# Optimization experiments

Hardware: AMD Instinct MI355X
Metric: run time of the kernel (lower is better)

## Reference

```python
import jax, jax.numpy as jnp
import numpy as np

B, L, D_MODEL = 2, 2048, 2048
D_INNER, D_STATE, D_CONV, DT_RANK = 4096, 16, 4, 128


def setup_inputs() -> dict:
    key = jax.random.key(0)
    ks = jax.random.split(key, 8)
    s = 0.02
    return {
        "hidden_states": jax.random.normal(ks[0], (B, L, D_MODEL), jnp.float32),
        "in_proj_weight": jax.random.normal(ks[1], (2 * D_INNER, D_MODEL), jnp.float32) * s,
        "conv1d_weight": jax.random.normal(ks[2], (D_INNER, 1, D_CONV), jnp.float32) * s,
        "conv1d_bias": jnp.zeros((D_INNER,), jnp.float32),
        "x_proj_weight": jax.random.normal(ks[3], (DT_RANK + 2 * D_STATE, D_INNER), jnp.float32) * s,
        "dt_proj_weight": jax.random.normal(ks[4], (D_INNER, DT_RANK), jnp.float32) * s,
        "dt_proj_bias": jax.random.uniform(ks[5], (D_INNER,), jnp.float32, -4.0, -2.0),
        "out_proj_weight": jax.random.normal(ks[6], (D_MODEL, D_INNER), jnp.float32) * s,
        # real Mamba init: A_log = log(1..d_state) broadcast over channels
        "A_log": jnp.log(jnp.broadcast_to(jnp.arange(1, D_STATE + 1, dtype=jnp.float32), (D_INNER, D_STATE))),
        "D": jnp.ones((D_INNER,), jnp.float32),
    }


def reference(hidden_states, in_proj_weight, conv1d_weight, conv1d_bias,
              x_proj_weight, dt_proj_weight, dt_proj_bias, out_proj_weight,
              A_log, D):
    negA = -jnp.exp(A_log)  # [d_inner, d_state]
    # in_proj (no bias) then transpose(1,2): [B, 2*d_inner, L]
    xz = jnp.einsum('bld,ed->bel', hidden_states, in_proj_weight)
    x, z = jnp.split(xz, 2, axis=1)  # each [B, d_inner, L]
    # causal depthwise conv1d + silu
    x = jax.lax.conv_general_dilated(
        x, conv1d_weight, window_strides=(1,), padding=[(D_CONV - 1, 0)],
        dimension_numbers=('NCH', 'OIH', 'NCH'), feature_group_count=D_INNER,
    ) + conv1d_bias[None, :, None]
    x = jax.nn.silu(x)
    xT = x.transpose(0, 2, 1)  # [B, L, d_inner]
    # x_proj -> (dt_rank, d_state, d_state)
    x_dbl = jnp.einsum('bld,ed->ble', xT, x_proj_weight)
    dt_lo = x_dbl[..., :DT_RANK]
    Bm = x_dbl[..., DT_RANK:DT_RANK + D_STATE]   # [B, L, n]
    Cm = x_dbl[..., DT_RANK + D_STATE:]          # [B, L, n]
    # dt_proj + delta_bias, softplus (delta_softplus=True)
    dt = jax.nn.softplus(jnp.einsum('blr,dr->bld', dt_lo, dt_proj_weight) + dt_proj_bias)

    # selective scan: h_t = exp(dt_t*A)*h_{t-1} + dt_t*x_t*B_t ; y_t = C_t . h_t
    def step(h, inp):
        dt_t, B_t, C_t, x_t = inp  # [B,d],[B,n],[B,n],[B,d]
        dA = jnp.exp(dt_t[..., None] * negA)           # [B, d, n]
        h = h * dA + (dt_t * x_t)[..., None] * B_t[:, None, :]
        y = jnp.einsum('bdn,bn->bd', h, C_t)
        return h, y

    h0 = jnp.zeros((B, D_INNER, D_STATE), dt.dtype)
    _, ys = jax.lax.scan(
        step, h0,
        (dt.transpose(1, 0, 2), Bm.transpose(1, 0, 2),
         Cm.transpose(1, 0, 2), xT.transpose(1, 0, 2)),
    )  # ys: [L, B, d_inner]
    y = ys.transpose(1, 0, 2) + xT * D          # skip connection D*x
    y = y * jax.nn.silu(z.transpose(0, 2, 1))   # gate
    # out_proj (no bias): [B, L, d_model]
    return jnp.einsum('bld,ed->ble', y, out_proj_weight)
```

## Files before the change

kernel.cpp:

```cpp
#include <hip/hip_runtime.h>
#include <math.h>

#define B_ 2
#define L_ 2048
#define DMODEL 2048
#define DINNER 4096
#define DSTATE 16
#define DCONV 4
#define DTRANK 128
#define NCHUNK 32
#define CLEN 64
#define MROWS 4096

typedef unsigned short ushort_t;
typedef unsigned int uint_t;
typedef __attribute__((ext_vector_type(8))) short bf16x8;
typedef __attribute__((ext_vector_type(4))) float floatx4;

__device__ __forceinline__ float sigmoidf_(float x){ return 1.f/(1.f+__expf(-x)); }
__device__ __forceinline__ ushort_t f2bf(float f){
    uint_t u = __builtin_bit_cast(uint_t, f);
    return (ushort_t)((u + 0x7FFFu + ((u >> 16) & 1u)) >> 16);
}
__device__ __forceinline__ float bf2f(ushort_t h){
    return __builtin_bit_cast(float, (uint_t)h << 16);
}
__device__ __forceinline__ float fast_exp2(float x){
#if __has_builtin(__builtin_amdgcn_exp2f)
    return __builtin_amdgcn_exp2f(x);
#else
    return exp2f(x);
#endif
}
#define LOG2E 1.44269504088896f

#define GLD_LDS16(g, l) __builtin_amdgcn_global_load_lds( \
    (const __attribute__((address_space(1))) void*)(g),   \
    (__attribute__((address_space(3))) void*)(l), 16, 0, 0)

template<int OUTBF, int EPI, int SPLIT, int KSPLIT>
__global__ __launch_bounds__(256)
void gemm_mfma(const ushort_t* __restrict__ Aptr, int lda,
               const ushort_t* __restrict__ W, int ldw,
               void* __restrict__ Cptr, void* __restrict__ C2,
               int ldc, int Klen,
               const float* __restrict__ bias)
{
    __shared__ ushort_t lsA[128*64];
    __shared__ ushort_t lsW[128*64];
    const int tid  = threadIdx.x;
    const int row0 = blockIdx.x * 128;
    const int col0 = blockIdx.y * 128;
    const int koff = KSPLIT ? blockIdx.z * Klen : 0;
    const int lane = tid & 63;
    const int wv   = tid >> 6;
    const int wm   = (wv >> 1) * 64;
    const int wn   = (wv & 1) * 64;
    const int lr   = lane & 15;
    const int lq   = lane >> 4;

    floatx4 acc[4][4];
    #pragma unroll
    for(int i=0;i<4;i++)
        #pragma unroll
        for(int j=0;j<4;j++)
            #pragma unroll
            for(int r=0;r<4;r++) acc[i][j][r] = 0.f;

    for(int k0 = koff; k0 < koff + Klen; k0 += 64){
        #pragma unroll
        for(int it=0; it<4; it++){
            const int slot = it*256 + tid;
            const int row  = slot >> 3;
            const int p    = slot & 7;
            const int s    = p ^ (row & 7);
            const ushort_t* gw = W    + (size_t)(col0 + row)*ldw + k0 + s*8;
            const ushort_t* ga = Aptr + (size_t)(row0 + row)*lda + k0 + s*8;
            GLD_LDS16(gw, &lsW[slot*8]);
            GLD_LDS16(ga, &lsA[slot*8]);
        }
        __syncthreads();

        #pragma unroll
        for(int kk=0; kk<2; kk++){
            bf16x8 af[4], bw[4];
            #pragma unroll
            for(int i=0;i<4;i++){
                const int ra = wm + i*16 + lr;
                const int rb = wn + i*16 + lr;
                af[i] = *(const bf16x8*)&lsA[ra*64 + (((kk*4+lq) ^ (ra&7))*8)];
                bw[i] = *(const bf16x8*)&lsW[rb*64 + (((kk*4+lq) ^ (rb&7))*8)];
            }
            #pragma unroll
            for(int i=0;i<4;i++)
                #pragma unroll
                for(int j=0;j<4;j++)
                    acc[i][j] = __builtin_amdgcn_mfma_f32_16x16x32_bf16(af[i], bw[j], acc[i][j], 0, 0, 0);
        }
        __syncthreads();
    }

    void* dst = Cptr;
    int cbase = col0;
    if (SPLIT && col0 >= ldc){ dst = C2; cbase = col0 - ldc; }
    const size_t zoff = KSPLIT ? (size_t)blockIdx.z * MROWS * ldc : 0;

    #pragma unroll
    for(int i=0;i<4;i++){
        #pragma unroll
        for(int r=0;r<4;r++){
            const int row = row0 + wm + i*16 + lq*4 + r;
            #pragma unroll
            for(int j=0;j<4;j++){
                const int col = cbase + wn + j*16 + lr;
                float v = acc[i][j][r];
                if (EPI){
                    v += bias[col];
                    v = (v > 20.f) ? v : log1pf(expf(v));
                }
                if (OUTBF) ((ushort_t*)dst)[(size_t)row*ldc + col] = f2bf(v);
                else       ((float*)  dst)[zoff + (size_t)row*ldc + col] = v;
            }
        }
    }
}

__global__ __launch_bounds__(256)
void cvt_bf16(const float* __restrict__ in, ushort_t* __restrict__ out, int n4)
{
    const int i = blockIdx.x*256 + threadIdx.x;
    if (i < n4){
        float4 v = *(const float4*)(in + (size_t)i*4);
        union { ushort_t u[4]; uint2 q; } p;
        p.u[0]=f2bf(v.x); p.u[1]=f2bf(v.y); p.u[2]=f2bf(v.z); p.u[3]=f2bf(v.w);
        *(uint2*)(out + (size_t)i*4) = p.q;
    }
}

__global__ __launch_bounds__(256)
void cvt_pad256(const float* __restrict__ in, ushort_t* __restrict__ out)
{
    const int i = blockIdx.x*256 + threadIdx.x;
    const int row = i >> 10;
    const int c4  = i & 1023;
    union { ushort_t u[4]; uint2 q; } p;
    if (row < 160){
        float4 v = *(const float4*)(in + (size_t)row*4096 + c4*4);
        p.u[0]=f2bf(v.x); p.u[1]=f2bf(v.y); p.u[2]=f2bf(v.z); p.u[3]=f2bf(v.w);
    } else { p.u[0]=0; p.u[1]=0; p.u[2]=0; p.u[3]=0; }
    *(uint2*)(out + (size_t)i*4) = p.q;
}

__global__ __launch_bounds__(256)
void reduce_xproj(const float* __restrict__ P, float* __restrict__ xdbl,
                  ushort_t* __restrict__ dtlo)
{
    const int row = blockIdx.x;
    const int col = threadIdx.x;
    float s = 0.f;
    #pragma unroll
    for(int z=0; z<8; z++)
        s += P[(size_t)z*MROWS*256 + (size_t)row*256 + col];
    if (col < 160) xdbl[(size_t)row*160 + col] = s;
    if (col < DTRANK) dtlo[(size_t)row*DTRANK + col] = f2bf(s);
}

__global__ __launch_bounds__(256)
void conv_silu_bf(const ushort_t* __restrict__ xb, const float* __restrict__ w,
                  const float* __restrict__ bias, ushort_t* __restrict__ xc)
{
    const int gid = blockIdx.x*256 + threadIdx.x;
    const int d = gid & (DINNER-1);
    const int t = gid >> 12;
    const int l = t & (L_-1);
    float s = bias[d];
    #pragma unroll
    for(int j=0;j<DCONV;j++){
        const int ll = l - (DCONV-1) + j;
        if (ll >= 0)
            s = fmaf(bf2f(xb[(size_t)(t-(DCONV-1)+j)*DINNER + d]), w[d*DCONV+j], s);
    }
    xc[(size_t)t*DINNER + d] = f2bf(s * sigmoidf_(s));
}

__global__ __launch_bounds__(256)
void scan_phase1(const ushort_t* __restrict__ dt_bf,
                 const ushort_t* __restrict__ xconv,
                 const float* __restrict__ xdbl,
                 const float* __restrict__ A_log,
                 float* __restrict__ sc_h, float* __restrict__ sc_S)
{
    const int tid = threadIdx.x;
    const int d = blockIdx.x*256 + tid;
    const int chunk = blockIdx.y;
    const int b = blockIdx.z;
    const int l0 = chunk*CLEN;

    __shared__ float Bs[CLEN][DSTATE];
    for(int i=tid; i<CLEN*DSTATE; i+=256){
        const int row = i >> 4, n = i & 15;
        Bs[row][n] = xdbl[(size_t)(b*L_ + l0 + row)*160 + DTRANK + n];
    }
    float negA[DSTATE];
    #pragma unroll
    for(int n=0;n<DSTATE;n++) negA[n] = -expf(A_log[d*DSTATE + n]) * LOG2E;
    __syncthreads();

    float h[DSTATE], S[DSTATE];
    #pragma unroll
    for(int n=0;n<DSTATE;n++){ h[n]=0.f; S[n]=0.f; }

    size_t idx = (size_t)(b*L_ + l0)*DINNER + d;
    float dt_c = bf2f(dt_bf[idx]);
    float xv_c = bf2f(xconv[idx]);
    for(int l=0;l<CLEN;l++){
        float dt_n = 0.f, xv_n = 0.f;
        if (l+1 < CLEN){
            dt_n = bf2f(dt_bf[idx + DINNER]);
            xv_n = bf2f(xconv[idx + DINNER]);
        }
        const float dx = dt_c * xv_c;
        #pragma unroll
        for(int n=0;n<DSTATE;n++){
            const float t = dt_c * negA[n];
            S[n] += t;
            h[n] = fmaf(h[n], fast_exp2(t), dx*Bs[l][n]);
        }
        dt_c = dt_n; xv_c = xv_n;
        idx += DINNER;
    }
    const size_t o = (size_t)(b*NCHUNK + chunk)*DSTATE*DINNER + d;
    #pragma unroll
    for(int n=0;n<DSTATE;n++){
        sc_h[o + (size_t)n*DINNER] = h[n];
        sc_S[o + (size_t)n*DINNER] = S[n];
    }
}

__global__ __launch_bounds__(256)
void scan_phase2(float* __restrict__ sc_h, const float* __restrict__ sc_S)
{
    const int gid = blockIdx.x*256 + threadIdx.x;
    const int b = gid / (DSTATE*DINNER);
    const int rem = gid - b*DSTATE*DINNER;
    const size_t base = (size_t)b*NCHUNK*DSTATE*DINNER + rem;
    float H = 0.f;
    #pragma unroll
    for(int c=0;c<NCHUNK;c++){
        const size_t idx = base + (size_t)c*DSTATE*DINNER;
        const float he = sc_h[idx];
        const float S  = sc_S[idx];
        sc_h[idx] = H;
        H = fmaf(fast_exp2(S), H, he);
    }
}

__global__ __launch_bounds__(256)
void scan_phase3(const ushort_t* __restrict__ dt_bf,
                 const ushort_t* __restrict__ xconv,
                 const float* __restrict__ xdbl,
                 const ushort_t* __restrict__ z_bf,
                 const float* __restrict__ A_log,
                 const float* __restrict__ Dvec,
                 const float* __restrict__ sc_h,
                 ushort_t* __restrict__ y_bf)
{
    const int tid = threadIdx.x;
    const int d = blockIdx.x*256 + tid;
    const int chunk = blockIdx.y;
    const int b = blockIdx.z;
    const int l0 = chunk*CLEN;

    __shared__ float BCs[CLEN][2*DSTATE];
    for(int i=tid; i<CLEN*2*DSTATE; i+=256){
        const int row = i >> 5, c = i & 31;
        BCs[row][c] = xdbl[(size_t)(b*L_ + l0 + row)*160 + DTRANK + c];
    }
    float negA[DSTATE];
    #pragma unroll
    for(int n=0;n<DSTATE;n++) negA[n] = -expf(A_log[d*DSTATE + n]) * LOG2E;
    const float Dv = Dvec[d];
    float h[DSTATE];
    const size_t o = (size_t)(b*NCHUNK + chunk)*DSTATE*DINNER + d;
    #pragma unroll
    for(int n=0;n<DSTATE;n++) h[n] = sc_h[o + (size_t)n*DINNER];
    __syncthreads();

    size_t idx = (size_t)(b*L_ + l0)*DINNER + d;
    float dt_c = bf2f(dt_bf[idx]);
    float xv_c = bf2f(xconv[idx]);
    float zv_c = bf2f(z_bf[idx]);
    for(int l=0;l<CLEN;l++){
        float dt_n = 0.f, xv_n = 0.f, zv_n = 0.f;
        if (l+1 < CLEN){
            dt_n = bf2f(dt_bf[idx + DINNER]);
            xv_n = bf2f(xconv[idx + DINNER]);
            zv_n = bf2f(z_bf[idx + DINNER]);
        }
        const float dx = dt_c * xv_c;
        float y = 0.f;
        #pragma unroll
        for(int n=0;n<DSTATE;n++){
            const float t = dt_c * negA[n];
            h[n] = fmaf(h[n], fast_exp2(t), dx*BCs[l][n]);
            y = fmaf(h[n], BCs[l][DSTATE+n], y);
        }
        const float g = zv_c * sigmoidf_(zv_c);
        y_bf[idx] = f2bf(fmaf(xv_c, Dv, y) * g);
        dt_c = dt_n; xv_c = xv_n; zv_c = zv_n;
        idx += DINNER;
    }
}

extern "C" void kernel_launch(void* const* d_in, const int* in_sizes, int n_in,
                              void* d_out, int out_size, void* d_ws, size_t ws_size,
                              hipStream_t stream) {
    const float* hs      = (const float*)d_in[0];
    const float* w_in    = (const float*)d_in[1];
    const float* w_conv  = (const float*)d_in[2];
    const float* b_conv  = (const float*)d_in[3];
    const float* w_xproj = (const float*)d_in[4];
    const float* w_dt    = (const float*)d_in[5];
    const float* b_dt    = (const float*)d_in[6];
    const float* w_out   = (const float*)d_in[7];
    const float* A_log   = (const float*)d_in[8];
    const float* Dvec    = (const float*)d_in[9];
    float* out = (float*)d_out;

    char* base = (char*)d_ws;
    ushort_t* x_bf   = (ushort_t*)(base);
    float*    xdbl   = (float*)   (base);
    ushort_t* wx_bf  = (ushort_t*)(base + (4u<<20));
    ushort_t* dtlo_bf= (ushort_t*)(base + (6u<<20));
    ushort_t* wdt_bf = (ushort_t*)(base + (7u<<20));
    float*    sc_h   = (float*)   (base + (8u<<20));
    ushort_t* z_bf   = (ushort_t*)(base + (32u<<20));
    ushort_t* xconv  = (ushort_t*)(base + (64u<<20));
    ushort_t* wi_bf  = (ushort_t*)(base + (96u<<20));
    ushort_t* dt_bf  = (ushort_t*)(base + (96u<<20));
    ushort_t* hs_bf  = (ushort_t*)(base + (128u<<20));
    float*    sc_S   = (float*)   (base + (128u<<20));
    ushort_t* wo_bf  = (ushort_t*)(base + (128u<<20));
    float*    xp_par = (float*)   (base + (144u<<20));
    ushort_t* y_bf   = (ushort_t*)(base + (144u<<20));

    dim3 blk(256);

    cvt_bf16<<<dim3(MROWS*DMODEL/4/256), blk, 0, stream>>>(hs, hs_bf, MROWS*DMODEL/4);
    cvt_bf16<<<dim3(2*DINNER*DMODEL/4/256), blk, 0, stream>>>(w_in, wi_bf, 2*DINNER*DMODEL/4);

    gemm_mfma<1,0,1,0><<<dim3(MROWS/128, 2*DINNER/128), blk, 0, stream>>>(
        hs_bf, DMODEL, wi_bf, DMODEL, x_bf, z_bf, DINNER, DMODEL, nullptr);

    conv_silu_bf<<<dim3((size_t)MROWS*DINNER/256), blk, 0, stream>>>(x_bf, w_conv, b_conv, xconv);

    cvt_pad256<<<dim3(256*4096/4/256), blk, 0, stream>>>(w_xproj, wx_bf);
    gemm_mfma<0,0,0,1><<<dim3(MROWS/128, 2, 8), blk, 0, stream>>>(
        xconv, DINNER, wx_bf, DINNER, xp_par, nullptr, 256, DINNER/8, nullptr);
    reduce_xproj<<<dim3(MROWS), blk, 0, stream>>>(xp_par, xdbl, dtlo_bf);

    cvt_bf16<<<dim3(DINNER*DTRANK/4/256), blk, 0, stream>>>(w_dt, wdt_bf, DINNER*DTRANK/4);
    gemm_mfma<1,1,0,0><<<dim3(MROWS/128, DINNER/128), blk, 0, stream>>>(
        dtlo_bf, DTRANK, wdt_bf, DTRANK, dt_bf, nullptr, DINNER, DTRANK, b_dt);

    dim3 sgrid(DINNER/256, NCHUNK, B_);
    scan_phase1<<<sgrid, blk, 0, stream>>>(dt_bf, xconv, xdbl, A_log, sc_h, sc_S);
    scan_phase2<<<dim3(B_*DSTATE*DINNER/256), blk, 0, stream>>>(sc_h, sc_S);

    cvt_bf16<<<dim3(DMODEL*DINNER/4/256), blk, 0, stream>>>(w_out, wo_bf, DMODEL*DINNER/4);

    scan_phase3<<<sgrid, blk, 0, stream>>>(dt_bf, xconv, xdbl, z_bf, A_log, Dvec, sc_h, y_bf);

    gemm_mfma<0,0,0,0><<<dim3(MROWS/128, DMODEL/128), blk, 0, stream>>>(
        y_bf, DINNER, wo_bf, DINNER, out, nullptr, DMODEL, DINNER, nullptr);
}
```

Before: 669.7 us.

## Use 256x256-tile 512-thread MFMA GEMM for in_proj and split-K out_proj

Adds a new GEMM kernel with 256x256 output tiles, 512 threads, double-buffered direct global-to-LDS loads, swizzled LDS layout and priority-boosted MFMA phases. It replaces the 128x128 GEMM for in_proj and for out_proj. The out_proj uses split-K by 2 into a float partial buffer, followed by a reduction kernel. The aim is more data reuse per tile and better latency hiding. In exchange it adds register pressure, an extra partial-sum write and read for out_proj, and one more launch.

```diff
diff --git a/kernel.cpp b/kernel.cpp
--- a/kernel.cpp
+++ b/kernel.cpp
@@ -125,6 +125,175 @@
     }
 }
 
+template<int OUTBF, int SPLIT, int KSPLIT>
+__global__ __launch_bounds__(512, 2)
+void gemm_256(const ushort_t* __restrict__ Aptr, int lda,
+              const ushort_t* __restrict__ W, int ldw,
+              void* __restrict__ Cptr, void* __restrict__ C2,
+              int ldc, int Klen)
+{
+    __shared__ ushort_t lds[2][2][2][8192];
+    const int tid  = threadIdx.x;
+    const int row0 = blockIdx.x * 256;
+    const int col0 = blockIdx.y * 256;
+    const int koff = KSPLIT ? blockIdx.z * Klen : 0;
+    const int NT   = Klen >> 6;
+    const int lane = tid & 63;
+    const int wv   = tid >> 6;
+    const int wr   = wv >> 2;
+    const int wc   = wv & 3;
+    const int lr   = lane & 15;
+    const int lq   = lane >> 4;
+
+    int sdst0, sdst1;
+    const ushort_t *aS0, *aS1, *wS0, *wS1;
+    {
+        const int g0 = tid,     dr0 = g0 >> 3, f0 = g0 & 7;
+        const int g1 = 512+tid, dr1 = g1 >> 3, f1 = g1 & 7;
+        const int u0 = f0 ^ (dr0 & 7), u1 = f1 ^ (dr1 & 7);
+        const int r0s = dr0*2 + (u0 >> 2), c0s = (u0 & 3)*8;
+        const int r1s = dr1*2 + (u1 >> 2), c1s = (u1 & 3)*8;
+        sdst0 = g0*8; sdst1 = g1*8;
+        aS0 = Aptr + (size_t)(row0 + r0s)*lda + c0s;
+        aS1 = Aptr + (size_t)(row0 + r1s)*lda + c1s;
+        wS0 = W    + (size_t)(col0 + r0s)*ldw + c0s;
+        wS1 = W    + (size_t)(col0 + r1s)*ldw + c1s;
+    }
+    #define STG_A(kc, reg) { GLD_LDS16(aS0 + (kc), &(reg)[sdst0]); \
+                             GLD_LDS16(aS1 + (kc), &(reg)[sdst1]); }
+    #define STG_W(kc, reg) { GLD_LDS16(wS0 + (kc), &(reg)[sdst0]); \
+                             GLD_LDS16(wS1 + (kc), &(reg)[sdst1]); }
+
+    const int frd = ((lr & 1)*4 + lq) ^ (lr >> 1);
+    const int aA  = (wr*64 + (lr >> 1))*64 + frd*8;
+    const int aB  = (wc*32 + (lr >> 1))*64 + frd*8;
+
+    floatx4 acc[8][4];
+    #pragma unroll
+    for(int i=0;i<8;i++)
+        #pragma unroll
+        for(int j=0;j<4;j++)
+            #pragma unroll
+            for(int r=0;r<4;r++) acc[i][j][r] = 0.f;
+
+    STG_A(koff,    lds[0][0][0]);
+    STG_W(koff,    lds[0][1][0]);
+    STG_A(koff+32, lds[0][0][1]);
+    STG_W(koff+32, lds[0][1][1]);
+    STG_A(koff+64, lds[1][0][0]);
+    STG_W(koff+64, lds[1][1][0]);
+    asm volatile("s_waitcnt vmcnt(8)\ns_barrier" ::: "memory");
+
+    for(int t=0; t<NT; ++t){
+        const int c = t & 1;
+        const ushort_t* LA0 = lds[c][0][0];
+        const ushort_t* LB0 = lds[c][1][0];
+        const ushort_t* LA1 = lds[c][0][1];
+        const ushort_t* LB1 = lds[c][1][1];
+        const int kt1 = koff + (t+1)*64;
+        const int kt2 = koff + (t+2)*64;
+        bf16x8 af[8], b0, b1;
+
+        #pragma unroll
+        for(int i=0;i<8;i++) af[i] = *(const bf16x8*)&LA0[aA + i*512];
+        b0 = *(const bf16x8*)&LB0[aB];
+        b1 = *(const bf16x8*)&LB0[aB + 512];
+        if (t+1 < NT) STG_A(kt1+32, lds[c^1][0][1]);
+        __builtin_amdgcn_s_barrier();
+        asm volatile("s_waitcnt lgkmcnt(0)" ::: "memory");
+        __builtin_amdgcn_s_setprio(1);
+        #pragma unroll
+        for(int i=0;i<8;i++){
+            acc[i][0] = __builtin_amdgcn_mfma_f32_16x16x32_bf16(af[i], b0, acc[i][0],0,0,0);
+            acc[i][1] = __builtin_amdgcn_mfma_f32_16x16x32_bf16(af[i], b1, acc[i][1],0,0,0);
+        }
+        __builtin_amdgcn_s_setprio(0);
+        __builtin_amdgcn_s_barrier();
+
+        b0 = *(const bf16x8*)&LB0[aB + 1024];
+        b1 = *(const bf16x8*)&LB0[aB + 1536];
+        if (t+1 < NT) STG_W(kt1+32, lds[c^1][1][1]);
+        __builtin_amdgcn_s_barrier();
+        asm volatile("s_waitcnt lgkmcnt(0)" ::: "memory");
+        __builtin_amdgcn_s_setprio(1);
+        #pragma unroll
+        for(int i=0;i<8;i++){
+            acc[i][2] = __builtin_amdgcn_mfma_f32_16x16x32_bf16(af[i], b0, acc[i][2],0,0,0);
+            acc[i][3] = __builtin_amdgcn_mfma_f32_16x16x32_bf16(af[i], b1, acc[i][3],0,0,0);
+        }
+        __builtin_amdgcn_s_setprio(0);
+        if (t+1 < NT) asm volatile("s_waitcnt vmcnt(8)\ns_barrier" ::: "memory");
+        else          asm volatile("s_waitcnt vmcnt(0)\ns_barrier" ::: "memory");
+
+        #pragma unroll
+        for(int i=0;i<8;i++) af[i] = *(const bf16x8*)&LA1[aA + i*512];
+        b0 = *(const bf16x8*)&LB1[aB];
+        b1 = *(const bf16x8*)&LB1[aB + 512];
+        if (t+2 < NT) STG_A(kt2, lds[c][0][0]);
+        __builtin_amdgcn_s_barrier();
+        asm volatile("s_waitcnt lgkmcnt(0)" ::: "memory");
+        __builtin_amdgcn_s_setprio(1);
+        #pragma unroll
+        for(int i=0;i<8;i++){
+            acc[i][0] = __builtin_amdgcn_mfma_f32_16x16x32_bf16(af[i], b0, acc[i][0],0,0,0);
+            acc[i][1] = __builtin_amdgcn_mfma_f32_16x16x32_bf16(af[i], b1, acc[i][1],0,0,0);
+        }
+        __builtin_amdgcn_s_setprio(0);
+        __builtin_amdgcn_s_barrier();
+
+        b0 = *(const bf16x8*)&LB1[aB + 1024];
+        b1 = *(const bf16x8*)&LB1[aB + 1536];
+        if (t+2 < NT) STG_W(kt2, lds[c][1][0]);
+        __builtin_amdgcn_s_barrier();
+        asm volatile("s_waitcnt lgkmcnt(0)" ::: "memory");
+        __builtin_amdgcn_s_setprio(1);
+        #pragma unroll
+        for(int i=0;i<8;i++){
+            acc[i][2] = __builtin_amdgcn_mfma_f32_16x16x32_bf16(af[i], b0, acc[i][2],0,0,0);
+            acc[i][3] = __builtin_amdgcn_mfma_f32_16x16x32_bf16(af[i], b1, acc[i][3],0,0,0);
+        }
+        __builtin_amdgcn_s_setprio(0);
+        if (t+2 < NT)      asm volatile("s_waitcnt vmcnt(8)\ns_barrier" ::: "memory");
+        else if (t+1 < NT) asm volatile("s_waitcnt vmcnt(4)\ns_barrier" ::: "memory");
+        else               asm volatile("s_barrier" ::: "memory");
+    }
+    #undef STG_A
+    #undef STG_W
+
+    void* dst = Cptr;
+    int cb = col0;
+    if (SPLIT && col0 >= ldc){ dst = C2; cb = col0 - ldc; }
+    const size_t zoff = KSPLIT ? (size_t)blockIdx.z * MROWS * ldc : 0;
+    const int rbase = row0 + wr*128 + lq*4;
+    const int cbase = cb + wc*64 + lr;
+    #pragma unroll
+    for(int i=0;i<8;i++){
+        #pragma unroll
+        for(int r=0;r<4;r++){
+            const int row = rbase + i*16 + r;
+            #pragma unroll
+            for(int j=0;j<4;j++){
+                const int col = cbase + j*16;
+                const float v = acc[i][j][r];
+                if (OUTBF) ((ushort_t*)dst)[(size_t)row*ldc + col] = f2bf(v);
+                else       ((float*)dst)[zoff + (size_t)row*ldc + col] = v;
+            }
+        }
+    }
+}
+
+__global__ __launch_bounds__(256)
+void reduce2(const float* __restrict__ P, float* __restrict__ out, int n4)
+{
+    const int i = blockIdx.x*256 + threadIdx.x;
+    if (i < n4){
+        float4 a = *(const float4*)(P + (size_t)i*4);
+        float4 b = *(const float4*)(P + (size_t)(i + n4)*4);
+        float4 r; r.x=a.x+b.x; r.y=a.y+b.y; r.z=a.z+b.z; r.w=a.w+b.w;
+        *(float4*)(out + (size_t)i*4) = r;
+    }
+}
+
 __global__ __launch_bounds__(256)
 void cvt_bf16(const float* __restrict__ in, ushort_t* __restrict__ out, int n4)
 {
@@ -335,6 +504,7 @@
     ushort_t* wdt_bf = (ushort_t*)(base + (7u<<20));
     float*    sc_h   = (float*)   (base + (8u<<20));
     ushort_t* z_bf   = (ushort_t*)(base + (32u<<20));
+    float*    op_par = (float*)   (base + (32u<<20));
     ushort_t* xconv  = (ushort_t*)(base + (64u<<20));
     ushort_t* wi_bf  = (ushort_t*)(base + (96u<<20));
     ushort_t* dt_bf  = (ushort_t*)(base + (96u<<20));
@@ -345,12 +515,13 @@
     ushort_t* y_bf   = (ushort_t*)(base + (144u<<20));
 
     dim3 blk(256);
+    dim3 blk5(512);
 
     cvt_bf16<<<dim3(MROWS*DMODEL/4/256), blk, 0, stream>>>(hs, hs_bf, MROWS*DMODEL/4);
     cvt_bf16<<<dim3(2*DINNER*DMODEL/4/256), blk, 0, stream>>>(w_in, wi_bf, 2*DINNER*DMODEL/4);
 
-    gemm_mfma<1,0,1,0><<<dim3(MROWS/128, 2*DINNER/128), blk, 0, stream>>>(
-        hs_bf, DMODEL, wi_bf, DMODEL, x_bf, z_bf, DINNER, DMODEL, nullptr);
+    gemm_256<1,1,0><<<dim3(MROWS/256, 2*DINNER/256), blk5, 0, stream>>>(
+        hs_bf, DMODEL, wi_bf, DMODEL, x_bf, z_bf, DINNER, DMODEL);
 
     conv_silu_bf<<<dim3((size_t)MROWS*DINNER/256), blk, 0, stream>>>(x_bf, w_conv, b_conv, xconv);
 
@@ -371,6 +542,7 @@
 
     scan_phase3<<<sgrid, blk, 0, stream>>>(dt_bf, xconv, xdbl, z_bf, A_log, Dvec, sc_h, y_bf);
 
-    gemm_mfma<0,0,0,0><<<dim3(MROWS/128, DMODEL/128), blk, 0, stream>>>(
-        y_bf, DINNER, wo_bf, DINNER, out, nullptr, DMODEL, DINNER, nullptr);
-}
+    gemm_256<0,0,1><<<dim3(MROWS/256, DMODEL/256, 2), blk5, 0, stream>>>(
+        y_bf, DINNER, wo_bf, DINNER, op_par, nullptr, DMODEL, DINNER/2);
+    reduce2<<<dim3(MROWS*DMODEL/4/256), blk, 0, stream>>>(op_par, out, MROWS*DMODEL/4);
+}
```

Result: slower. 685.6 us (+2.4%).

## Add 256x256-tile 1024-thread GEMM with triple-buffered LDS for in_proj

Applied to the files above, without the earlier changes.

Introduces a new bf16 MFMA GEMM kernel using 256x256 output tiles, 16 waves per block and a three-stage LDS ring fed by direct global-to-LDS loads, and uses it for the in_proj GEMM. Larger tiles raise arithmetic intensity and cut global traffic per FLOP, and the deeper prefetch is meant to hide load latency. The in_proj grid shrinks to 16x32 blocks, which may limit occupancy and leave some CUs idle. The large LDS footprint (96KB) and register pressure from the 64 accumulators per thread add further occupancy risk.

```diff
diff --git a/kernel.cpp b/kernel.cpp
--- a/kernel.cpp
+++ b/kernel.cpp
@@ -120,6 +120,99 @@
                 }
                 if (OUTBF) ((ushort_t*)dst)[(size_t)row*ldc + col] = f2bf(v);
                 else       ((float*)  dst)[zoff + (size_t)row*ldc + col] = v;
+            }
+        }
+    }
+}
+
+template<int OUTBF, int SPLIT, int KSPLIT>
+__global__ __launch_bounds__(1024, 4)
+void gemm_256w(const ushort_t* __restrict__ Aptr, int lda,
+               const ushort_t* __restrict__ W, int ldw,
+               void* __restrict__ Cptr, void* __restrict__ C2,
+               int ldc, int Klen)
+{
+    __shared__ ushort_t lds[3][2][8192];
+    const int tid  = threadIdx.x;
+    const int row0 = blockIdx.x * 256;
+    const int col0 = blockIdx.y * 256;
+    const int koff = KSPLIT ? blockIdx.z * Klen : 0;
+    const int NT   = Klen >> 5;
+    const int lane = tid & 63;
+    const int wv   = tid >> 6;
+    const int wr   = wv >> 2;
+    const int wc   = wv & 3;
+    const int lr   = lane & 15;
+    const int lq   = lane >> 4;
+
+    const int srow = tid >> 2;
+    const int sc   = (tid & 3) ^ ((srow >> 1) & 3);
+    const ushort_t* aS = Aptr + (size_t)(row0 + srow)*lda + sc*8;
+    const ushort_t* wS = W    + (size_t)(col0 + srow)*ldw + sc*8;
+    const int sdst = tid*8;
+
+    const int rA = wr*64 + lr;
+    const int rB = wc*64 + lr;
+    const int aA = rA*32 + ((lq ^ ((rA>>1)&3))*8);
+    const int aB = rB*32 + ((lq ^ ((rB>>1)&3))*8);
+
+    floatx4 acc[4][4];
+    #pragma unroll
+    for(int i=0;i<4;i++)
+        #pragma unroll
+        for(int j=0;j<4;j++)
+            #pragma unroll
+            for(int r=0;r<4;r++) acc[i][j][r] = 0.f;
+
+    GLD_LDS16(aS + koff,      &lds[0][0][sdst]);
+    GLD_LDS16(wS + koff,      &lds[0][1][sdst]);
+    GLD_LDS16(aS + koff + 32, &lds[1][0][sdst]);
+    GLD_LDS16(wS + koff + 32, &lds[1][1][sdst]);
+
+    int bs = 0;
+    for(int t=0; t<NT; ++t){
+        if (t+1 < NT) asm volatile("s_waitcnt vmcnt(2)\ns_barrier" ::: "memory");
+        else          asm volatile("s_waitcnt vmcnt(0)\ns_barrier" ::: "memory");
+        const ushort_t* pA = lds[bs][0];
+        const ushort_t* pB = lds[bs][1];
+        bf16x8 af[4], bw[4];
+        #pragma unroll
+        for(int j=0;j<4;j++) bw[j] = *(const bf16x8*)&pB[aB + j*512];
+        #pragma unroll
+        for(int i=0;i<4;i++) af[i] = *(const bf16x8*)&pA[aA + i*512];
+        if (t+2 < NT){
+            int b2 = bs + 2; if (b2 >= 3) b2 -= 3;
+            const int kc = koff + (t+2)*32;
+            GLD_LDS16(aS + kc, &lds[b2][0][sdst]);
+            GLD_LDS16(wS + kc, &lds[b2][1][sdst]);
+        }
+        __builtin_amdgcn_s_setprio(1);
+        #pragma unroll
+        for(int i=0;i<4;i++)
+            #pragma unroll
+            for(int j=0;j<4;j++)
+                acc[i][j] = __builtin_amdgcn_mfma_f32_16x16x32_bf16(af[i], bw[j], acc[i][j],0,0,0);
+        __builtin_amdgcn_s_setprio(0);
+        bs = (bs + 1 == 3) ? 0 : bs + 1;
+    }
+
+    void* dst = Cptr;
+    int cb = col0;
+    if (SPLIT && col0 >= ldc){ dst = C2; cb = col0 - ldc; }
+    const size_t zoff = KSPLIT ? (size_t)blockIdx.z * MROWS * ldc : 0;
+    const int rbase = row0 + wr*64 + lq*4;
+    const int cbase = cb + wc*64 + lr;
+    #pragma unroll
+    for(int i=0;i<4;i++){
+        #pragma unroll
+        for(int r=0;r<4;r++){
+            const int row = rbase + i*16 + r;
+            #pragma unroll
+            for(int j=0;j<4;j++){
+                const int col = cbase + j*16;
+                const float v = acc[i][j][r];
+                if (OUTBF) ((ushort_t*)dst)[(size_t)row*ldc + col] = f2bf(v);
+                else       ((float*)dst)[zoff + (size_t)row*ldc + col] = v;
             }
         }
     }
@@ -345,12 +438,13 @@
     ushort_t* y_bf   = (ushort_t*)(base + (144u<<20));
 
     dim3 blk(256);
+    dim3 blkW(1024);
 
     cvt_bf16<<<dim3(MROWS*DMODEL/4/256), blk, 0, stream>>>(hs, hs_bf, MROWS*DMODEL/4);
     cvt_bf16<<<dim3(2*DINNER*DMODEL/4/256), blk, 0, stream>>>(w_in, wi_bf, 2*DINNER*DMODEL/4);
 
-    gemm_mfma<1,0,1,0><<<dim3(MROWS/128, 2*DINNER/128), blk, 0, stream>>>(
-        hs_bf, DMODEL, wi_bf, DMODEL, x_bf, z_bf, DINNER, DMODEL, nullptr);
+    gemm_256w<1,1,0><<<dim3(MROWS/256, 2*DINNER/256), blkW, 0, stream>>>(
+        hs_bf, DMODEL, wi_bf, DMODEL, x_bf, z_bf, DINNER, DMODEL);
 
     conv_silu_bf<<<dim3((size_t)MROWS*DINNER/256), blk, 0, stream>>>(x_bf, w_conv, b_conv, xconv);
 
```

Result: slower. 689.0 us (+2.9%).
